# Kernel tuning notes

Measured on AMD Instinct MI355X. Metric: run time of the kernel, lower is better.

Reference implementation:

```python
import jax, jax.numpy as jnp
import numpy as np

N_NODES = 100000


def _gcn_norm(edge_index, num_nodes):
    # add self loops
    src, dst = edge_index[0], edge_index[1]
    loop = jnp.arange(num_nodes, dtype=src.dtype)
    row = jnp.concatenate([src, loop])  # [E+N]
    col = jnp.concatenate([dst, loop])
    ew = jnp.ones(row.shape[0], dtype=jnp.float32)
    deg = jax.ops.segment_sum(ew, col, num_segments=num_nodes)  # [N]
    dinv = jnp.where(deg > 0, jax.lax.rsqrt(deg), 0.0)
    norm = dinv[row] * ew * dinv[col]  # [E+N]
    return row, col, norm


def setup_inputs() -> dict:
    key = jax.random.key(0)
    k1, k2, k3 = jax.random.split(key, 3)
    x = jax.random.normal(k1, (N_NODES, 64), dtype=jnp.float32)
    edge_index = jax.random.randint(k2, (2, 1280000), 0, N_NODES, dtype=jnp.int64)
    W = jax.random.normal(k3, (40, 64), dtype=jnp.float32) * (1.0 / np.sqrt(64))
    b = jnp.zeros((40,), dtype=jnp.float32)
    return {"x": x, "edge_index": edge_index, "W": W, "b": b}


def reference(x, edge_index, W, b):
    K = 3
    row, col, norm = _gcn_norm(edge_index, N_NODES)
    h = x
    for _ in range(K):
        # gather from source nodes, scale by symmetric norm, scatter-add to dst
        msg = norm[:, None] * h[row]  # [E+N, F]
        h = jax.ops.segment_sum(msg, col, num_segments=N_NODES)
    logits = h @ W.T + b  # [N, C]
    return jax.nn.log_softmax(logits, axis=1)
```

## Files before the change

### kernel.cpp

```cpp
#include <hip/hip_runtime.h>

#define F_IN 64
#define F_OUT 40
#define USTRIDE 20
#define QPN 5

#define PART_BLK 256
#define PART_EPB 16
#define PART_TILE (PART_BLK * PART_EPB)
#define BSHIFT 8
#define BCAP 4096
#define MAXB 512

#define WSTRIDE 17

__device__ inline unsigned pk2(float x, float y) {
    unsigned a = __float_as_uint(x); a = (a + 0x7FFFu + ((a >> 16) & 1u)) >> 16;
    unsigned b = __float_as_uint(y); b = (b + 0x7FFFu + ((b >> 16) & 1u)) >> 16;
    return a | (b << 16);
}
__device__ inline void up2(unsigned u, float& a, float& b) {
    a = __uint_as_float(u << 16); b = __uint_as_float(u & 0xFFFF0000u);
}

__global__ __launch_bounds__(PART_BLK) void partition_kernel(const int* __restrict__ src,
                                                             const int* __restrict__ dst,
                                                             int* __restrict__ bfill,
                                                             unsigned* __restrict__ staging,
                                                             int E, int nbk) {
    __shared__ int hist[MAXB];
    __shared__ int base[MAXB];
    int tid = threadIdx.x;
    for (int b = tid; b < nbk; b += PART_BLK) hist[b] = 0;
    __syncthreads();

    int rank[PART_EPB];
    int bk[PART_EPB];
    unsigned rec[PART_EPB];
    int eb = blockIdx.x * PART_TILE + tid;
#pragma unroll
    for (int k = 0; k < PART_EPB; ++k) {
        int e = eb + k * PART_BLK;
        if (e < E) {
            int r = src[e];
            int c = dst[e];
            int b = c >> BSHIFT;
            bk[k] = b;
            rec[k] = (unsigned)r | ((unsigned)(c & 255) << 17);
            rank[k] = atomicAdd(&hist[b], 1);
        } else {
            bk[k] = -1;
        }
    }
    __syncthreads();
    for (int b = tid; b < nbk; b += PART_BLK) {
        int h = hist[b];
        base[b] = h ? (b * BCAP + atomicAdd(&bfill[b], h)) : 0;
    }
    __syncthreads();
#pragma unroll
    for (int k = 0; k < PART_EPB; ++k) {
        if (bk[k] >= 0) staging[base[bk[k]] + rank[k]] = rec[k];
    }
}

__global__ __launch_bounds__(512) void btotal_scan_kernel(const int* __restrict__ bfill,
                                                          int* __restrict__ ebase,
                                                          int* __restrict__ rowptr_end,
                                                          int nbk, int E) {
    __shared__ int s[512];
    int tid = threadIdx.x;
    int v = (tid < nbk) ? bfill[tid] : 0;
    s[tid] = v;
    __syncthreads();
    for (int off = 1; off < 512; off <<= 1) {
        int t = (tid >= off) ? s[tid - off] : 0;
        __syncthreads();
        s[tid] += t;
        __syncthreads();
    }
    if (tid < nbk) ebase[tid] = s[tid] - v;
    if (tid == 0) *rowptr_end = E;
}

__global__ __launch_bounds__(256) void bucket_finalize_kernel(const unsigned* __restrict__ staging,
                                                              const int* __restrict__ bfill,
                                                              const int* __restrict__ ebase,
                                                              int* __restrict__ rowptr,
                                                              int* __restrict__ deg,
                                                              float* __restrict__ dinv,
                                                              float* __restrict__ dinv2,
                                                              int* __restrict__ srcs,
                                                              int* __restrict__ perm, int n) {
    int b = blockIdx.x;
    __shared__ int h[256];
    __shared__ int cur[256];
    __shared__ unsigned keys[256];
    int tid = threadIdx.x;
    h[tid] = 0;
    __syncthreads();

    int cnt = bfill[b];
    const unsigned* rec = staging + (size_t)b * BCAP;
    for (int i = tid; i < cnt; i += 256) {
        atomicAdd(&h[rec[i] >> 17], 1);
    }
    __syncthreads();

    int v = h[tid];
    keys[tid] = ((unsigned)v << 8) | (unsigned)(255 - tid);

    for (int off = 1; off < 256; off <<= 1) {
        int t = (tid >= off) ? h[tid - off] : 0;
        __syncthreads();
        h[tid] += t;
        __syncthreads();
    }
    int excl = h[tid] - v;
    int base = ebase[b];
    int node = (b << BSHIFT) | tid;
    if (node < n) {
        rowptr[node] = base + excl;
        deg[node] = v;
        float r = rsqrtf((float)v + 1.0f);
        dinv[node] = r;
        dinv2[node] = r * r;
    }
    cur[tid] = base + excl;
    __syncthreads();

    for (int i = tid; i < cnt; i += 256) {
        unsigned rv = rec[i];
        int pos = atomicAdd(&cur[rv >> 17], 1);
        srcs[pos] = (int)(rv & 0x1FFFFu);
    }
    __syncthreads();

    for (int k = 2; k <= 256; k <<= 1) {
        for (int j = k >> 1; j > 0; j >>= 1) {
            int p = tid ^ j;
            if (p > tid) {
                unsigned a = keys[tid];
                unsigned c = keys[p];
                bool asc_region = ((tid & k) == 0);
                if (asc_region ? (a < c) : (a > c)) {
                    keys[tid] = c;
                    keys[p] = a;
                }
            }
            __syncthreads();
        }
    }
    perm[(b << BSHIFT) | tid] = (b << BSHIFT) | (int)(255u - (keys[tid] & 255u));
}

__global__ __launch_bounds__(256, 4) void proj_kernel(const float* __restrict__ x,
                                                      const float* __restrict__ W,
                                                      const float* __restrict__ dinv,
                                                      unsigned* __restrict__ u, int n) {
    __shared__ float Ws[F_OUT * WSTRIDE * 4];
    for (int i = threadIdx.x; i < F_OUT * F_IN; i += 256) {
        int c = i >> 6;
        int k = i & 63;
        Ws[c * (WSTRIDE * 4) + k] = W[i];
    }
    __syncthreads();

    int t = blockIdx.x * 256 + threadIdx.x;
    int g = t >> 2;
    int q = t & 3;
    int n0 = 2 * g;
    if (n0 >= n) return;
    int n1 = n0 + 1;

    const float4* xp0 = (const float4*)(x + (size_t)n0 * F_IN);
    const float4* xp1 = (const float4*)(x + (size_t)n1 * F_IN);
    const float4* Wq  = (const float4*)Ws + (size_t)(q * 10) * WSTRIDE;

    float acc0[10], acc1[10];
#pragma unroll
    for (int c = 0; c < 10; ++c) { acc0[c] = 0.0f; acc1[c] = 0.0f; }

#pragma unroll 1
    for (int f4 = 0; f4 < F_IN / 4; ++f4) {
        float4 x0 = xp0[f4];
        float4 x1 = xp1[f4];
#pragma unroll
        for (int c = 0; c < 10; ++c) {
            float4 w = Wq[c * WSTRIDE + f4];
            acc0[c] += x0.x * w.x + x0.y * w.y + x0.z * w.z + x0.w * w.w;
            acc1[c] += x1.x * w.x + x1.y * w.y + x1.z * w.z + x1.w * w.w;
        }
    }

    float d0 = dinv[n0];
    float d1 = dinv[n1];
    unsigned* up0 = u + (size_t)n0 * USTRIDE + q * 5;
    unsigned* up1 = u + (size_t)n1 * USTRIDE + q * 5;
#pragma unroll
    for (int j = 0; j < 5; ++j) {
        up0[j] = pk2(d0 * acc0[2 * j], d0 * acc0[2 * j + 1]);
        up1[j] = pk2(d1 * acc1[2 * j], d1 * acc1[2 * j + 1]);
    }
}

__global__ __launch_bounds__(256) void propagate_kernel(const int* __restrict__ perm,
                                                        const int* __restrict__ rowptr,
                                                        const int* __restrict__ srcs,
                                                        const float* __restrict__ dinv2,
                                                        const unsigned* __restrict__ ucur,
                                                        unsigned* __restrict__ unew, int n) {
    int t = blockIdx.x * blockDim.x + threadIdx.x;
    int g = t / QPN;
    int q = t - g * QPN;
    if (g >= n) return;
    int node = perm[g];

    int beg = rowptr[node];
    int end = rowptr[node + 1];

    const uint4* U = (const uint4*)ucur;
    uint4 sv = U[(size_t)node * QPN + q];
    float a0, a1, a2, a3, a4, a5, a6, a7;
    up2(sv.x, a0, a1); up2(sv.y, a2, a3); up2(sv.z, a4, a5); up2(sv.w, a6, a7);

    int i = beg;
    for (; i + 3 < end; i += 4) {
        int s0 = srcs[i], s1 = srcs[i + 1], s2 = srcs[i + 2], s3 = srcs[i + 3];
        uint4 v0 = U[(size_t)s0 * QPN + q];
        uint4 v1 = U[(size_t)s1 * QPN + q];
        uint4 v2 = U[(size_t)s2 * QPN + q];
        uint4 v3 = U[(size_t)s3 * QPN + q];
        float b0, b1;
        up2(v0.x, b0, b1); a0 += b0; a1 += b1;
        up2(v0.y, b0, b1); a2 += b0; a3 += b1;
        up2(v0.z, b0, b1); a4 += b0; a5 += b1;
        up2(v0.w, b0, b1); a6 += b0; a7 += b1;
        up2(v1.x, b0, b1); a0 += b0; a1 += b1;
        up2(v1.y, b0, b1); a2 += b0; a3 += b1;
        up2(v1.z, b0, b1); a4 += b0; a5 += b1;
        up2(v1.w, b0, b1); a6 += b0; a7 += b1;
        up2(v2.x, b0, b1); a0 += b0; a1 += b1;
        up2(v2.y, b0, b1); a2 += b0; a3 += b1;
        up2(v2.z, b0, b1); a4 += b0; a5 += b1;
        up2(v2.w, b0, b1); a6 += b0; a7 += b1;
        up2(v3.x, b0, b1); a0 += b0; a1 += b1;
        up2(v3.y, b0, b1); a2 += b0; a3 += b1;
        up2(v3.z, b0, b1); a4 += b0; a5 += b1;
        up2(v3.w, b0, b1); a6 += b0; a7 += b1;
    }
    for (; i < end; ++i) {
        uint4 v = U[(size_t)srcs[i] * QPN + q];
        float b0, b1;
        up2(v.x, b0, b1); a0 += b0; a1 += b1;
        up2(v.y, b0, b1); a2 += b0; a3 += b1;
        up2(v.z, b0, b1); a4 += b0; a5 += b1;
        up2(v.w, b0, b1); a6 += b0; a7 += b1;
    }

    float ds = dinv2[node];
    uint4 o;
    o.x = pk2(ds * a0, ds * a1);
    o.y = pk2(ds * a2, ds * a3);
    o.z = pk2(ds * a4, ds * a5);
    o.w = pk2(ds * a6, ds * a7);
    ((uint4*)unew)[(size_t)node * QPN + q] = o;
}

__global__ void logsoftmax_kernel(const unsigned* __restrict__ u, float* __restrict__ out,
                                  const float* __restrict__ bias,
                                  const int* __restrict__ deg, int n) {
    int node = blockIdx.x * blockDim.x + threadIdx.x;
    if (node >= n) return;
    float sq = sqrtf((float)deg[node] + 1.0f);
    const uint4* up = (const uint4*)(u + (size_t)node * USTRIDE);
    float v[F_OUT];
#pragma unroll
    for (int g = 0; g < 5; ++g) {
        uint4 t = up[g];
        float a, b2;
        up2(t.x, a, b2); v[8 * g + 0] = sq * a + bias[8 * g + 0];
                         v[8 * g + 1] = sq * b2 + bias[8 * g + 1];
        up2(t.y, a, b2); v[8 * g + 2] = sq * a + bias[8 * g + 2];
                         v[8 * g + 3] = sq * b2 + bias[8 * g + 3];
        up2(t.z, a, b2); v[8 * g + 4] = sq * a + bias[8 * g + 4];
                         v[8 * g + 5] = sq * b2 + bias[8 * g + 5];
        up2(t.w, a, b2); v[8 * g + 6] = sq * a + bias[8 * g + 6];
                         v[8 * g + 7] = sq * b2 + bias[8 * g + 7];
    }
    float mx = -1e30f;
#pragma unroll
    for (int c = 0; c < F_OUT; ++c) mx = fmaxf(mx, v[c]);
    float se = 0.0f;
#pragma unroll
    for (int c = 0; c < F_OUT; ++c) se += __expf(v[c] - mx);
    float lse = mx + __logf(se);
    float4* p = (float4*)(out + (size_t)node * F_OUT);
#pragma unroll
    for (int c4 = 0; c4 < F_OUT / 4; ++c4) {
        float4 t;
        t.x = v[4 * c4 + 0] - lse; t.y = v[4 * c4 + 1] - lse;
        t.z = v[4 * c4 + 2] - lse; t.w = v[4 * c4 + 3] - lse;
        p[c4] = t;
    }
}

extern "C" void kernel_launch(void* const* d_in, const int* in_sizes, int n_in,
                              void* d_out, int out_size, void* d_ws, size_t ws_size,
                              hipStream_t stream) {
    const float* x  = (const float*)d_in[0];
    const int*   ei = (const int*)d_in[1];
    const float* W  = (const float*)d_in[2];
    const float* b  = (const float*)d_in[3];

    const int N = in_sizes[0] / F_IN;
    const int E = in_sizes[1] / 2;
    const int* src = ei;
    const int* dst = ei + E;
    const int nbk = (N + (1 << BSHIFT) - 1) >> BSHIFT;

    char* base = (char*)d_ws;
    size_t off = 0;
    auto alloc = [&](size_t bytes) {
        char* p = base + off;
        off = (off + bytes + 255) & ~(size_t)255;
        return p;
    };
    int*      deg_i   = (int*)     alloc((size_t)N * 4);
    float*    dinv    = (float*)   alloc((size_t)N * 4);
    float*    dinv2   = (float*)   alloc((size_t)N * 4);
    int*      rowptr  = (int*)     alloc((size_t)(N + 1) * 4);
    int*      bfill   = (int*)     alloc((size_t)MAXB * 4);
    int*      ebase   = (int*)     alloc((size_t)MAXB * 4);
    int*      perm    = (int*)     alloc((size_t)(nbk << BSHIFT) * 4);
    unsigned* staging = (unsigned*)alloc((size_t)nbk * BCAP * 4);
    int*      srcs_s  = (int*)     alloc((size_t)E * 4);
    unsigned* uA      = (unsigned*)alloc((size_t)N * USTRIDE * 4);
    unsigned* uB      = (unsigned*)alloc((size_t)N * USTRIDE * 4);
    float*    outp    = (float*)d_out;

    hipMemsetAsync(bfill, 0, (size_t)nbk * 4, stream);
    partition_kernel<<<(E + PART_TILE - 1) / PART_TILE, PART_BLK, 0, stream>>>(
        src, dst, bfill, staging, E, nbk);

    btotal_scan_kernel<<<1, 512, 0, stream>>>(bfill, ebase, rowptr + N, nbk, E);
    bucket_finalize_kernel<<<nbk, 256, 0, stream>>>(staging, bfill, ebase, rowptr,
                                                    deg_i, dinv, dinv2, srcs_s, perm, N);

    proj_kernel<<<((size_t)N * 2 + 255) / 256, 256, 0, stream>>>(x, W, dinv, uA, N);

    const int pt = N * QPN;
    const int pg = (pt + 255) / 256;
    propagate_kernel<<<pg, 256, 0, stream>>>(perm, rowptr, srcs_s, dinv2, uA, uB, N);
    propagate_kernel<<<pg, 256, 0, stream>>>(perm, rowptr, srcs_s, dinv2, uB, uA, N);
    propagate_kernel<<<pg, 256, 0, stream>>>(perm, rowptr, srcs_s, dinv2, uA, uB, N);

    logsoftmax_kernel<<<(N + 255) / 256, 256, 0, stream>>>(uB, outp, b, deg_i, N);
}
```

Baseline: 245.1 us.

## Fuse final propagation with log-softmax and drop degree-sorted node permutation

The third propagation pass is merged with the bias add and log-softmax. Five threads per node reduce max and sum-exp through shared memory, which removes one kernel launch and the bf16 write and re-read of the final features. The bitonic sort that built a degree-ordered permutation is removed, so propagation processes nodes in natural order. This gives up the load balancing the sort provided and skips that sort work and the perm indirection. The fused kernel leaves 1 of 256 threads idle per block (51 nodes × 5).

```diff
diff --git a/kernel.cpp b/kernel.cpp
--- a/kernel.cpp
+++ b/kernel.cpp
@@ -13,6 +13,7 @@
 #define MAXB 512
 
 #define WSTRIDE 17
+#define NPB 51
 
 __device__ inline unsigned pk2(float x, float y) {
     unsigned a = __float_as_uint(x); a = (a + 0x7FFFu + ((a >> 16) & 1u)) >> 16;
@@ -87,15 +88,12 @@
                                                               const int* __restrict__ bfill,
                                                               const int* __restrict__ ebase,
                                                               int* __restrict__ rowptr,
-                                                              int* __restrict__ deg,
                                                               float* __restrict__ dinv,
                                                               float* __restrict__ dinv2,
-                                                              int* __restrict__ srcs,
-                                                              int* __restrict__ perm, int n) {
+                                                              int* __restrict__ srcs, int n) {
     int b = blockIdx.x;
     __shared__ int h[256];
     __shared__ int cur[256];
-    __shared__ unsigned keys[256];
     int tid = threadIdx.x;
     h[tid] = 0;
     __syncthreads();
@@ -108,8 +106,6 @@
     __syncthreads();
 
     int v = h[tid];
-    keys[tid] = ((unsigned)v << 8) | (unsigned)(255 - tid);
-
     for (int off = 1; off < 256; off <<= 1) {
         int t = (tid >= off) ? h[tid - off] : 0;
         __syncthreads();
@@ -121,7 +117,6 @@
     int node = (b << BSHIFT) | tid;
     if (node < n) {
         rowptr[node] = base + excl;
-        deg[node] = v;
         float r = rsqrtf((float)v + 1.0f);
         dinv[node] = r;
         dinv2[node] = r * r;
@@ -134,24 +129,6 @@
         int pos = atomicAdd(&cur[rv >> 17], 1);
         srcs[pos] = (int)(rv & 0x1FFFFu);
     }
-    __syncthreads();
-
-    for (int k = 2; k <= 256; k <<= 1) {
-        for (int j = k >> 1; j > 0; j >>= 1) {
-            int p = tid ^ j;
-            if (p > tid) {
-                unsigned a = keys[tid];
-                unsigned c = keys[p];
-                bool asc_region = ((tid & k) == 0);
-                if (asc_region ? (a < c) : (a > c)) {
-                    keys[tid] = c;
-                    keys[p] = a;
-                }
-            }
-            __syncthreads();
-        }
-    }
-    perm[(b << BSHIFT) | tid] = (b << BSHIFT) | (int)(255u - (keys[tid] & 255u));
 }
 
 __global__ __launch_bounds__(256, 4) void proj_kernel(const float* __restrict__ x,
@@ -204,17 +181,15 @@
     }
 }
 
-__global__ __launch_bounds__(256) void propagate_kernel(const int* __restrict__ perm,
-                                                        const int* __restrict__ rowptr,
+__global__ __launch_bounds__(256) void propagate_kernel(const int* __restrict__ rowptr,
                                                         const int* __restrict__ srcs,
                                                         const float* __restrict__ dinv2,
                                                         const unsigned* __restrict__ ucur,
                                                         unsigned* __restrict__ unew, int n) {
     int t = blockIdx.x * blockDim.x + threadIdx.x;
-    int g = t / QPN;
-    int q = t - g * QPN;
-    if (g >= n) return;
-    int node = perm[g];
+    int node = t / QPN;
+    int q = t - node * QPN;
+    if (node >= n) return;
 
     int beg = rowptr[node];
     int end = rowptr[node + 1];
@@ -267,41 +242,94 @@
     ((uint4*)unew)[(size_t)node * QPN + q] = o;
 }
 
-__global__ void logsoftmax_kernel(const unsigned* __restrict__ u, float* __restrict__ out,
-                                  const float* __restrict__ bias,
-                                  const int* __restrict__ deg, int n) {
-    int node = blockIdx.x * blockDim.x + threadIdx.x;
-    if (node >= n) return;
-    float sq = sqrtf((float)deg[node] + 1.0f);
-    const uint4* up = (const uint4*)(u + (size_t)node * USTRIDE);
-    float v[F_OUT];
-#pragma unroll
-    for (int g = 0; g < 5; ++g) {
-        uint4 t = up[g];
-        float a, b2;
-        up2(t.x, a, b2); v[8 * g + 0] = sq * a + bias[8 * g + 0];
-                         v[8 * g + 1] = sq * b2 + bias[8 * g + 1];
-        up2(t.y, a, b2); v[8 * g + 2] = sq * a + bias[8 * g + 2];
-                         v[8 * g + 3] = sq * b2 + bias[8 * g + 3];
-        up2(t.z, a, b2); v[8 * g + 4] = sq * a + bias[8 * g + 4];
-                         v[8 * g + 5] = sq * b2 + bias[8 * g + 5];
-        up2(t.w, a, b2); v[8 * g + 6] = sq * a + bias[8 * g + 6];
-                         v[8 * g + 7] = sq * b2 + bias[8 * g + 7];
-    }
-    float mx = -1e30f;
-#pragma unroll
-    for (int c = 0; c < F_OUT; ++c) mx = fmaxf(mx, v[c]);
-    float se = 0.0f;
-#pragma unroll
-    for (int c = 0; c < F_OUT; ++c) se += __expf(v[c] - mx);
+__global__ __launch_bounds__(256) void propagate_lsm_kernel(const int* __restrict__ rowptr,
+                                                            const int* __restrict__ srcs,
+                                                            const float* __restrict__ dinv,
+                                                            const unsigned* __restrict__ ucur,
+                                                            const float* __restrict__ bias,
+                                                            float* __restrict__ out, int n) {
+    __shared__ float red[256];
+    int tid = threadIdx.x;
+    int gl = tid / QPN;
+    int q  = tid - gl * QPN;
+    int node = blockIdx.x * NPB + gl;
+    bool active = (gl < NPB) && (node < n);
+
+    float a0 = 0, a1 = 0, a2 = 0, a3 = 0, a4 = 0, a5 = 0, a6 = 0, a7 = 0;
+    float dv = 0.0f;
+    if (active) {
+        int beg = rowptr[node];
+        int end = rowptr[node + 1];
+        const uint4* U = (const uint4*)ucur;
+        uint4 sv = U[(size_t)node * QPN + q];
+        up2(sv.x, a0, a1); up2(sv.y, a2, a3); up2(sv.z, a4, a5); up2(sv.w, a6, a7);
+        int i = beg;
+        for (; i + 3 < end; i += 4) {
+            int s0 = srcs[i], s1 = srcs[i + 1], s2 = srcs[i + 2], s3 = srcs[i + 3];
+            uint4 v0 = U[(size_t)s0 * QPN + q];
+            uint4 v1 = U[(size_t)s1 * QPN + q];
+            uint4 v2 = U[(size_t)s2 * QPN + q];
+            uint4 v3 = U[(size_t)s3 * QPN + q];
+            float b0, b1;
+            up2(v0.x, b0, b1); a0 += b0; a1 += b1;
+            up2(v0.y, b0, b1); a2 += b0; a3 += b1;
+            up2(v0.z, b0, b1); a4 += b0; a5 += b1;
+            up2(v0.w, b0, b1); a6 += b0; a7 += b1;
+            up2(v1.x, b0, b1); a0 += b0; a1 += b1;
+            up2(v1.y, b0, b1); a2 += b0; a3 += b1;
+            up2(v1.z, b0, b1); a4 += b0; a5 += b1;
+            up2(v1.w, b0, b1); a6 += b0; a7 += b1;
+            up2(v2.x, b0, b1); a0 += b0; a1 += b1;
+            up2(v2.y, b0, b1); a2 += b0; a3 += b1;
+            up2(v2.z, b0, b1); a4 += b0; a5 += b1;
+            up2(v2.w, b0, b1); a6 += b0; a7 += b1;
+            up2(v3.x, b0, b1); a0 += b0; a1 += b1;
+            up2(v3.y, b0, b1); a2 += b0; a3 += b1;
+            up2(v3.z, b0, b1); a4 += b0; a5 += b1;
+            up2(v3.w, b0, b1); a6 += b0; a7 += b1;
+        }
+        for (; i < end; ++i) {
+            uint4 v = U[(size_t)srcs[i] * QPN + q];
+            float b0, b1;
+            up2(v.x, b0, b1); a0 += b0; a1 += b1;
+            up2(v.y, b0, b1); a2 += b0; a3 += b1;
+            up2(v.z, b0, b1); a4 += b0; a5 += b1;
+            up2(v.w, b0, b1); a6 += b0; a7 += b1;
+        }
+        dv = dinv[node];
+    }
+
+    float y0 = dv * a0 + bias[q * 8 + 0];
+    float y1 = dv * a1 + bias[q * 8 + 1];
+    float y2 = dv * a2 + bias[q * 8 + 2];
+    float y3 = dv * a3 + bias[q * 8 + 3];
+    float y4 = dv * a4 + bias[q * 8 + 4];
+    float y5 = dv * a5 + bias[q * 8 + 5];
+    float y6 = dv * a6 + bias[q * 8 + 6];
+    float y7 = dv * a7 + bias[q * 8 + 7];
+
+    float pm = fmaxf(fmaxf(fmaxf(y0, y1), fmaxf(y2, y3)),
+                     fmaxf(fmaxf(y4, y5), fmaxf(y6, y7)));
+    red[tid] = active ? pm : -1e30f;
+    __syncthreads();
+    int base = tid - q;
+    float mx = fmaxf(fmaxf(fmaxf(red[base], red[base + 1]), fmaxf(red[base + 2], red[base + 3])),
+                     red[base + 4]);
+    __syncthreads();
+    float ps = __expf(y0 - mx) + __expf(y1 - mx) + __expf(y2 - mx) + __expf(y3 - mx)
+             + __expf(y4 - mx) + __expf(y5 - mx) + __expf(y6 - mx) + __expf(y7 - mx);
+    red[tid] = active ? ps : 0.0f;
+    __syncthreads();
+    float se = red[base] + red[base + 1] + red[base + 2] + red[base + 3] + red[base + 4];
     float lse = mx + __logf(se);
-    float4* p = (float4*)(out + (size_t)node * F_OUT);
-#pragma unroll
-    for (int c4 = 0; c4 < F_OUT / 4; ++c4) {
-        float4 t;
-        t.x = v[4 * c4 + 0] - lse; t.y = v[4 * c4 + 1] - lse;
-        t.z = v[4 * c4 + 2] - lse; t.w = v[4 * c4 + 3] - lse;
-        p[c4] = t;
+
+    if (active) {
+        float4* p = (float4*)(out + (size_t)node * F_OUT + q * 8);
+        float4 o0, o1;
+        o0.x = y0 - lse; o0.y = y1 - lse; o0.z = y2 - lse; o0.w = y3 - lse;
+        o1.x = y4 - lse; o1.y = y5 - lse; o1.z = y6 - lse; o1.w = y7 - lse;
+        p[0] = o0;
+        p[1] = o1;
     }
 }
 
@@ -326,13 +354,11 @@
         off = (off + bytes + 255) & ~(size_t)255;
         return p;
     };
-    int*      deg_i   = (int*)     alloc((size_t)N * 4);
     float*    dinv    = (float*)   alloc((size_t)N * 4);
     float*    dinv2   = (float*)   alloc((size_t)N * 4);
     int*      rowptr  = (int*)     alloc((size_t)(N + 1) * 4);
     int*      bfill   = (int*)     alloc((size_t)MAXB * 4);
     int*      ebase   = (int*)     alloc((size_t)MAXB * 4);
-    int*      perm    = (int*)     alloc((size_t)(nbk << BSHIFT) * 4);
     unsigned* staging = (unsigned*)alloc((size_t)nbk * BCAP * 4);
     int*      srcs_s  = (int*)     alloc((size_t)E * 4);
     unsigned* uA      = (unsigned*)alloc((size_t)N * USTRIDE * 4);
@@ -345,15 +371,15 @@
 
     btotal_scan_kernel<<<1, 512, 0, stream>>>(bfill, ebase, rowptr + N, nbk, E);
     bucket_finalize_kernel<<<nbk, 256, 0, stream>>>(staging, bfill, ebase, rowptr,
-                                                    deg_i, dinv, dinv2, srcs_s, perm, N);
+                                                    dinv, dinv2, srcs_s, N);
 
     proj_kernel<<<((size_t)N * 2 + 255) / 256, 256, 0, stream>>>(x, W, dinv, uA, N);
 
     const int pt = N * QPN;
     const int pg = (pt + 255) / 256;
-    propagate_kernel<<<pg, 256, 0, stream>>>(perm, rowptr, srcs_s, dinv2, uA, uB, N);
-    propagate_kernel<<<pg, 256, 0, stream>>>(perm, rowptr, srcs_s, dinv2, uB, uA, N);
-    propagate_kernel<<<pg, 256, 0, stream>>>(perm, rowptr, srcs_s, dinv2, uA, uB, N);
-
-    logsoftmax_kernel<<<(N + 255) / 256, 256, 0, stream>>>(uB, outp, b, deg_i, N);
-}
+    propagate_kernel<<<pg, 256, 0, stream>>>(rowptr, srcs_s, dinv2, uA, uB, N);
+    propagate_kernel<<<pg, 256, 0, stream>>>(rowptr, srcs_s, dinv2, uB, uA, N);
+
+    const int fb = (N + NPB - 1) / NPB;
+    propagate_lsm_kernel<<<fb, 256, 0, stream>>>(rowptr, srcs_s, dinv, uA, b, outp, N);
+}
```

New measurement: 212.0 us. 1.16x faster.
